# Kernel optimization log

Measured on AMD Instinct MI355X. Metric: run time of the kernel, lower is better.

## Reference

```python
import jax, jax.numpy as jnp
import numpy as np

D_MODEL = 256
NUM_LAYERS = 4
NUM_FREQ = 16
D_STATE = 8
NUM_HEADS = 4
LN_EPS = 1e-5


def setup_inputs() -> dict:
    key = jax.random.key(0)
    ks = jax.random.split(key, 30)
    B, NS, NQ = 16, 1024, 1024
    D, L, S = D_MODEL, NUM_LAYERS, D_STATE
    cin = 2 * NUM_FREQ + 1  # 33
    w = lambda k, shp, s=0.02: jax.random.normal(k, shp, dtype=jnp.float32) * s
    inp = {
        'sparse_coords': jax.random.uniform(ks[0], (B, NS, 2), minval=-1.0, maxval=1.0, dtype=jnp.float32),
        'sparse_values': jax.random.normal(ks[1], (B, NS, 1), dtype=jnp.float32),
        'query_coords': jax.random.uniform(ks[2], (B, NQ, 2), minval=-1.0, maxval=1.0, dtype=jnp.float32),
        't': jax.random.uniform(ks[3], (B,), dtype=jnp.float32),
        'noise': jax.random.normal(ks[4], (B, NQ, 1), dtype=jnp.float32),
        'B_f': jax.random.normal(ks[5], (2, NUM_FREQ), dtype=jnp.float32) * 10.0,
        'Wq_in': w(ks[6], (D, cin)), 'bq_in': jnp.zeros((D,), jnp.float32),
        'Wi_in': w(ks[7], (D, cin)), 'bi_in': jnp.zeros((D,), jnp.float32),
        'A_log': jax.random.normal(ks[8], (L, S), dtype=jnp.float32) * 0.1 - 1.0,
        'Bw': w(ks[9], (L, S, D)),
        'Cw': w(ks[10], (L, D, S)),
        'Dp': jax.random.normal(ks[11], (L, D), dtype=jnp.float32) * 0.01,
        'ln_g': jnp.ones((L, D), jnp.float32), 'ln_b': jnp.zeros((L, D), jnp.float32),
        'gate_w': w(ks[12], (L, D, D)), 'gate_b': jnp.zeros((L, D), jnp.float32),
        'in_proj_w': w(ks[13], (3 * D, D)), 'in_proj_b': jnp.zeros((3 * D,), jnp.float32),
        'out_w': w(ks[14], (D, D)), 'out_b': jnp.zeros((D,), jnp.float32),
        'dec_w1': w(ks[15], (D, D)), 'dec_b1': jnp.zeros((D,), jnp.float32),
        'dec_w2': w(ks[16], (1, D)), 'dec_b2': jnp.zeros((1,), jnp.float32),
    }
    return inp


def _layernorm(x, g, b):
    mu = jnp.mean(x, axis=-1, keepdims=True)
    var = jnp.mean(jnp.square(x - mu), axis=-1, keepdims=True)
    return (x - mu) * jax.lax.rsqrt(var + LN_EPS) * g + b


def _ssm(x, A_log, Bw, Cw, Dp):
    # x: (B, N, D)
    Bsz, N, D = x.shape
    A = -jnp.clip(jnp.exp(A_log), 1e-8, 10.0)          # (S,)
    A_bar = jnp.exp(A / N)                              # dt = 1/N
    Bu = jnp.einsum('bnd,sd->bns', x, Bw)               # (B, N, S)

    def step(h, bu_t):
        h = A_bar * h + bu_t
        return h, h

    h0 = jnp.zeros((Bsz, A_log.shape[0]), x.dtype)
    _, hs = jax.lax.scan(step, h0, jnp.swapaxes(Bu, 0, 1))  # (N, B, S)
    hs = jnp.swapaxes(hs, 0, 1)                             # (B, N, S)
    return jnp.einsum('bns,ds->bnd', hs, Cw) + Dp * x


def _time_embed(t, dim):
    half = dim // 2
    freqs = jnp.exp(jnp.arange(half, dtype=jnp.float32) * (-jnp.log(10000.0) / (half - 1)))
    emb = t[:, None] * freqs[None, :]
    return jnp.concatenate([jnp.sin(emb), jnp.cos(emb)], axis=-1)


def _fourier(coords, B_f):
    proj = coords @ B_f
    return jnp.concatenate([jnp.sin(proj), jnp.cos(proj)], axis=-1)


def reference(sparse_coords, sparse_values, query_coords, t, noise, B_f,
              Wq_in, bq_in, Wi_in, bi_in,
              A_log, Bw, Cw, Dp, ln_g, ln_b, gate_w, gate_b,
              in_proj_w, in_proj_b, out_w, out_b,
              dec_w1, dec_b1, dec_w2, dec_b2):
    D = D_MODEL
    NS = sparse_coords.shape[1]
    sparse_feats = _fourier(sparse_coords, B_f)
    query_feats = _fourier(query_coords, B_f)
    input_tokens = jnp.concatenate([sparse_feats, sparse_values], -1) @ Wi_in.T + bi_in
    query_tokens = jnp.concatenate([query_feats, noise], -1) @ Wq_in.T + bq_in
    t_emb = _time_embed(t, D)[:, None, :]
    seq = jnp.concatenate([input_tokens + t_emb, query_tokens + t_emb], axis=1)

    for l in range(A_log.shape[0]):
        xn = _layernorm(seq, ln_g[l], ln_b[l])
        gate = jax.nn.sigmoid(xn @ gate_w[l].T + gate_b[l])
        seq = seq + gate * _ssm(xn, A_log[l], Bw[l], Cw[l], Dp[l])

    input_seq = seq[:, :NS, :]
    query_seq = seq[:, NS:, :]

    # multi-head cross-attention (torch nn.MultiheadAttention semantics)
    H, hd = NUM_HEADS, D // NUM_HEADS
    q = query_seq @ in_proj_w[:D].T + in_proj_b[:D]
    k = input_seq @ in_proj_w[D:2 * D].T + in_proj_b[D:2 * D]
    v = input_seq @ in_proj_w[2 * D:].T + in_proj_b[2 * D:]
    def split(x):
        b, n, _ = x.shape
        return x.reshape(b, n, H, hd).transpose(0, 2, 1, 3)
    q, k, v = split(q), split(k), split(v)
    scores = jnp.einsum('bhqd,bhkd->bhqk', q, k) / jnp.sqrt(jnp.float32(hd))
    attn = jax.nn.softmax(scores, axis=-1)
    o = jnp.einsum('bhqk,bhkd->bhqd', attn, v)
    o = o.transpose(0, 2, 1, 3).reshape(query_seq.shape[0], -1, D)
    attended = o @ out_w.T + out_b

    h = jax.nn.relu(attended @ dec_w1.T + dec_b1)
    return h @ dec_w2.T + dec_b2
```

## Files before the change

kernel.cpp:

```cpp
#include <hip/hip_runtime.h>
#include <math.h>


typedef float floatx4 __attribute__((ext_vector_type(4)));
typedef short shortx8 __attribute__((ext_vector_type(8)));

__device__ __forceinline__ unsigned short f2bf(float f) {
  unsigned u = __builtin_bit_cast(unsigned, f);
  u += 0x7FFFu + ((u >> 16) & 1u);
  return (unsigned short)(u >> 16);
}
__device__ __forceinline__ float bf2f(unsigned short h) {
  unsigned u = ((unsigned)h) << 16;
  return __builtin_bit_cast(float, u);
}
__device__ __forceinline__ unsigned cvt_pk_bf16(float a, float b) {
  unsigned r;
  asm("v_cvt_pk_bf16_f32 %0, %1, %2" : "=v"(r) : "v"(a), "v"(b));
  return r;
}
__device__ __forceinline__ void split2(float f0, float f1, unsigned& ph, unsigned& pl) {
  ph = cvt_pk_bf16(f0, f1);
  float r0 = f0 - __builtin_bit_cast(float, ph << 16);
  float r1 = f1 - __builtin_bit_cast(float, ph & 0xFFFF0000u);
  pl = cvt_pk_bf16(r0, r1);
}
__device__ __forceinline__ void split8(float4 a, float4 b, uint4& uh, uint4& ul) {
  unsigned h0, h1, h2, h3, l0, l1, l2, l3;
  split2(a.x, a.y, h0, l0);
  split2(a.z, a.w, h1, l1);
  split2(b.x, b.y, h2, l2);
  split2(b.z, b.w, h3, l3);
  uh = make_uint4(h0, h1, h2, h3);
  ul = make_uint4(l0, l1, l2, l3);
}
__device__ __forceinline__ shortx8 lds_frag(const unsigned short* S, int row, int u) {
  uint4 v = *(const uint4*)(S + row * 64 + ((u ^ (row & 7)) << 3));
  return __builtin_bit_cast(shortx8, v);
}
__device__ __forceinline__ shortx8 lds_frag_v(const unsigned short* S, int row, int u) {
  uint4 v = *(const uint4*)(S + row * 64 + (((u ^ row ^ (row >> 3)) & 7) << 3));
  return __builtin_bit_cast(shortx8, v);
}
__device__ __forceinline__ shortx8 gfrag(const unsigned short* p) {
  return __builtin_bit_cast(shortx8, *(const uint4*)p);
}
__device__ __forceinline__ floatx4 mfma16(shortx8 a, shortx8 b, floatx4 c) {
  return __builtin_amdgcn_mfma_f32_16x16x32_bf16(a, b, c, 0, 0, 0);
}
__device__ __forceinline__ float wave_sum64(float v) {
#pragma unroll
  for (int m = 1; m < 64; m <<= 1) v += __shfl_xor(v, m);
  return v;
}

__global__ __launch_bounds__(256) void wconv_k(
    const float* __restrict__ gw, const float* __restrict__ ipw,
    const float* __restrict__ ow, const float* __restrict__ d1w,
    unsigned short* __restrict__ dh, unsigned short* __restrict__ dl) {
  int i = (blockIdx.x * 256 + threadIdx.x) * 8;
  const float* src;
  if (i < 262144) src = gw + i;
  else if (i < 458752) src = ipw + (i - 262144);
  else if (i < 524288) src = ow + (i - 458752);
  else src = d1w + (i - 524288);
  uint4 uh, ul;
  split8(*(const float4*)src, *(const float4*)(src + 4), uh, ul);
  *(uint4*)(dh + i) = uh;
  *(uint4*)(dl + i) = ul;
}

__global__ __launch_bounds__(256) void wconv2_k(
    const float* __restrict__ Wi, const float* __restrict__ Wq,
    unsigned short* __restrict__ eh, unsigned short* __restrict__ el) {
  int idx = blockIdx.x * 256 + threadIdx.x;
  int sel = idx >> 14, rem = idx & 16383;
  int row = rem >> 6, k = rem & 63;
  float v = 0.f;
  if (k < 33) v = (sel ? Wq : Wi)[row * 33 + k];
  unsigned short h = f2bf(v);
  eh[idx] = h;
  el[idx] = f2bf(v - bf2f(h));
}

__global__ __launch_bounds__(256) void embed_k(
    const float* __restrict__ sc, const float* __restrict__ sv,
    const float* __restrict__ qc, const float* __restrict__ tarr,
    const float* __restrict__ noise, const float* __restrict__ Bf,
    const float* __restrict__ bq, const float* __restrict__ bi,
    const unsigned short* __restrict__ Weh, const unsigned short* __restrict__ Wel,
    float* __restrict__ seq) {
  __shared__ unsigned short Ah[64 * 64];
  __shared__ unsigned short Al[64 * 64];
  __shared__ float teb[256];
  int tid = threadIdx.x;
  int bid = blockIdx.x;
  int chunk = bid & 15, half = (bid >> 4) & 1, b = bid >> 5;
  int rowbase = b * 2048 + half * 1024 + chunk * 64;
  {
    uint4 z = make_uint4(0, 0, 0, 0);
    *(uint4*)(Ah + tid * 8) = z;
    *(uint4*)(Ah + 2048 + tid * 8) = z;
    *(uint4*)(Al + tid * 8) = z;
    *(uint4*)(Al + 2048 + tid * 8) = z;
  }
  {
    float t = tarr[b];
    int dd = tid & 127;
    float e = t * __expf((float)dd * -0.07252236513367074f);
    float v = (tid < 128) ? sinf(e) : cosf(e);
    teb[tid] = v + (half ? bq : bi)[tid];
  }
  __syncthreads();
  {
    int tok = tid >> 2;
    int n = chunk * 64 + tok;
    const float* cp = (half ? qc : sc) + (size_t)(b * 1024 + n) * 2;
    float cx = cp[0], cy = cp[1];
#pragma unroll
    for (int jj = 0; jj < 4; ++jj) {
      int fr = (tid & 3) * 4 + jj;
      float px = cx * Bf[fr] + cy * Bf[16 + fr];
      float s = sinf(px), c = cosf(px);
      unsigned short sh = f2bf(s), ch = f2bf(c);
      int ks = fr, kc = 16 + fr;
      Ah[tok * 64 + (((ks >> 3) ^ (tok & 7)) << 3) + (ks & 7)] = sh;
      Al[tok * 64 + (((ks >> 3) ^ (tok & 7)) << 3) + (ks & 7)] = f2bf(s - bf2f(sh));
      Ah[tok * 64 + (((kc >> 3) ^ (tok & 7)) << 3) + (kc & 7)] = ch;
      Al[tok * 64 + (((kc >> 3) ^ (tok & 7)) << 3) + (kc & 7)] = f2bf(c - bf2f(ch));
    }
    if ((tid & 3) == 0) {
      float vv = (half ? noise : sv)[b * 1024 + n];
      unsigned short vh = f2bf(vv);
      Ah[tok * 64 + ((4 ^ (tok & 7)) << 3)] = vh;
      Al[tok * 64 + ((4 ^ (tok & 7)) << 3)] = f2bf(vv - bf2f(vh));
    }
  }
  __syncthreads();
  int w = tid >> 6, lane = tid & 63, lm = lane & 15, quad = lane >> 4;
  const unsigned short* Wb = Weh + half * 16384;
  const unsigned short* Wbl = Wel + half * 16384;
  floatx4 acc[4][4] = {};
#pragma unroll
  for (int s = 0; s < 2; ++s) {
    shortx8 afh[4], afl[4];
#pragma unroll
    for (int i = 0; i < 4; ++i) {
      afh[i] = lds_frag(Ah, i * 16 + lm, s * 4 + quad);
      afl[i] = lds_frag(Al, i * 16 + lm, s * 4 + quad);
    }
#pragma unroll
    for (int n = 0; n < 4; ++n) {
      int wr = w * 64 + n * 16 + lm;
      shortx8 bh = gfrag(Wb + wr * 64 + (s * 4 + quad) * 8);
      shortx8 bl = gfrag(Wbl + wr * 64 + (s * 4 + quad) * 8);
#pragma unroll
      for (int i = 0; i < 4; ++i) {
        acc[i][n] = mfma16(afl[i], bh, acc[i][n]);
        acc[i][n] = mfma16(afh[i], bl, acc[i][n]);
        acc[i][n] = mfma16(afh[i], bh, acc[i][n]);
      }
    }
  }
#pragma unroll
  for (int i = 0; i < 4; ++i)
#pragma unroll
    for (int n = 0; n < 4; ++n) {
      int col = w * 64 + n * 16 + lm;
      float te = teb[col];
#pragma unroll
      for (int r = 0; r < 4; ++r) {
        int tok = i * 16 + quad * 4 + r;
        seq[(size_t)(rowbase + tok) * 256 + col] = acc[i][n][r] + te;
      }
    }
}

__global__ __launch_bounds__(256) void scan_k(
    const float* __restrict__ BuT, const float* __restrict__ A_log,
    float* __restrict__ hsT) {
  int tid = threadIdx.x;
  int wid = blockIdx.x * 4 + (tid >> 6);
  int lane = tid & 63;
  int b = wid >> 3, s = wid & 7;
  float A = -fminf(fmaxf(expf(A_log[s]), 1e-8f), 10.0f);
  float abar = expf(A * (1.0f / 2048.0f));
  size_t base = (size_t)s * 32768 + b * 2048 + lane * 32;
  const float4* bu4 = (const float4*)(BuT + base);
  float4 v[8];
#pragma unroll
  for (int k = 0; k < 8; ++k) v[k] = bu4[k];
  float bl = 0.f;
#pragma unroll
  for (int k = 0; k < 8; ++k) {
    bl = abar * bl + v[k].x;
    bl = abar * bl + v[k].y;
    bl = abar * bl + v[k].z;
    bl = abar * bl + v[k].w;
  }
  float a = expf(A * (32.0f / 2048.0f));
  float bb = bl;
#pragma unroll
  for (int off = 1; off < 64; off <<= 1) {
    float pa = __shfl_up(a, (unsigned)off);
    float pb = __shfl_up(bb, (unsigned)off);
    if (lane >= off) { bb = a * pb + bb; a = a * pa; }
  }
  float h = __shfl_up(bb, 1u);
  if (lane == 0) h = 0.f;
  float4* hp4 = (float4*)(hsT + base);
#pragma unroll
  for (int k = 0; k < 8; ++k) {
    float h0 = abar * h + v[k].x;
    float h1 = abar * h0 + v[k].y;
    float h2 = abar * h1 + v[k].z;
    float h3 = abar * h2 + v[k].w;
    hp4[k] = make_float4(h0, h1, h2, h3);
    h = h3;
  }
}

template <int HASUPD>
__global__ __launch_bounds__(256, 2) void pe_k(
    float* __restrict__ seq, const float* __restrict__ Gprev,
    const float* __restrict__ hsTp, const float* __restrict__ CwP,
    const float* __restrict__ DpP, const float* __restrict__ gP,
    const float* __restrict__ bP, const float* __restrict__ gC,
    const float* __restrict__ bC, const float* __restrict__ BwL,
    const unsigned short* __restrict__ Wh, const unsigned short* __restrict__ Wl,
    const float* __restrict__ gbias, float* __restrict__ Gout,
    float* __restrict__ BuT) {
  __shared__ unsigned short slab[64 * 536];
  __shared__ float hsL[8 * 64];
  __shared__ float BwLds[8 * 256];
  int tid = threadIdx.x;
  int m0 = (int)blockIdx.x * 64;
  int w = tid >> 6, lane = tid & 63, lm = lane & 15, quad = lane >> 4;

#pragma unroll
  for (int j = 0; j < 8; ++j) BwLds[j * 256 + tid] = BwL[j * 256 + tid];
  if (HASUPD) {
    hsL[tid] = hsTp[(size_t)(tid >> 6) * 32768 + m0 + (tid & 63)];
    int v1 = tid + 256;
    hsL[v1] = hsTp[(size_t)(v1 >> 6) * 32768 + m0 + (v1 & 63)];
  }

  if (HASUPD) {
    __syncthreads();
    int c0 = lane * 4;
    float cw[4][8], dp4[4];
#pragma unroll
    for (int n = 0; n < 4; ++n) {
      float4 a0 = *(const float4*)(CwP + (size_t)(c0 + n) * 8);
      float4 a1 = *(const float4*)(CwP + (size_t)(c0 + n) * 8 + 4);
      cw[n][0] = a0.x; cw[n][1] = a0.y; cw[n][2] = a0.z; cw[n][3] = a0.w;
      cw[n][4] = a1.x; cw[n][5] = a1.y; cw[n][6] = a1.z; cw[n][7] = a1.w;
      dp4[n] = DpP[c0 + n];
    }
    float4 gg = *(const float4*)(gP + c0);
    float4 bb = *(const float4*)(bP + c0);
#pragma unroll
    for (int rr = 0; rr < 16; ++rr) {
      int r = w * 16 + rr;
      int row = m0 + r;
      float4 x = *(const float4*)(seq + (size_t)row * 256 + c0);
      float s1 = x.x + x.y + x.z + x.w;
      float s2 = x.x * x.x + x.y * x.y + x.z * x.z + x.w * x.w;
#pragma unroll
      for (int mk = 1; mk < 64; mk <<= 1) {
        s1 += __shfl_xor(s1, mk);
        s2 += __shfl_xor(s2, mk);
      }
      float mu = s1 * (1.0f / 256.0f);
      float var = s2 * (1.0f / 256.0f) - mu * mu;
      float rs = rsqrtf(var + 1e-5f);
      float xn0 = (x.x - mu) * rs * gg.x + bb.x;
      float xn1 = (x.y - mu) * rs * gg.y + bb.y;
      float xn2 = (x.z - mu) * rs * gg.z + bb.z;
      float xn3 = (x.w - mu) * rs * gg.w + bb.w;
      float hv[8];
#pragma unroll
      for (int s = 0; s < 8; ++s) hv[s] = hsL[s * 64 + r];
      float y0 = dp4[0] * xn0, y1 = dp4[1] * xn1, y2 = dp4[2] * xn2, y3 = dp4[3] * xn3;
#pragma unroll
      for (int s = 0; s < 8; ++s) {
        y0 += hv[s] * cw[0][s];
        y1 += hv[s] * cw[1][s];
        y2 += hv[s] * cw[2][s];
        y3 += hv[s] * cw[3][s];
      }
      float4 gp = *(const float4*)(Gprev + (size_t)row * 256 + c0);
      x.x += gp.x * y0; x.y += gp.y * y1; x.z += gp.z * y2; x.w += gp.w * y3;
      *(float4*)(seq + (size_t)row * 256 + c0) = x;
      *(float4*)((char*)slab + (size_t)r * 1072 + c0 * 4) = x;
    }
    __syncthreads();
  }

  {
    int r = tid >> 2, q2 = tid & 3;
    int row = m0 + r;
    float4 xr[16];
#pragma unroll
    for (int j = 0; j < 16; ++j) {
      if (HASUPD)
        xr[j] = *(const float4*)((const char*)slab + (size_t)r * 1072 + (q2 * 64 + j * 4) * 4);
      else
        xr[j] = *(const float4*)(seq + (size_t)row * 256 + q2 * 64 + j * 4);
    }
    __syncthreads();
    float s1 = 0.f, s2 = 0.f;
#pragma unroll
    for (int j = 0; j < 16; ++j) {
      s1 += (xr[j].x + xr[j].y) + (xr[j].z + xr[j].w);
      s2 += (xr[j].x * xr[j].x + xr[j].y * xr[j].y) + (xr[j].z * xr[j].z + xr[j].w * xr[j].w);
    }
    s1 += __shfl_xor(s1, 1); s2 += __shfl_xor(s2, 1);
    s1 += __shfl_xor(s1, 2); s2 += __shfl_xor(s2, 2);
    float mu = s1 * (1.0f / 256.0f);
    float var = s2 * (1.0f / 256.0f) - mu * mu;
    float rs = rsqrtf(var + 1e-5f);
    float bu[8] = {};
#pragma unroll
    for (int j = 0; j < 16; ++j) {
      int c = q2 * 64 + j * 4;
      float4 gg = *(const float4*)(gC + c);
      float4 bb = *(const float4*)(bC + c);
      float4 xn;
      xn.x = (xr[j].x - mu) * rs * gg.x + bb.x;
      xn.y = (xr[j].y - mu) * rs * gg.y + bb.y;
      xn.z = (xr[j].z - mu) * rs * gg.z + bb.z;
      xn.w = (xr[j].w - mu) * rs * gg.w + bb.w;
#pragma unroll
      for (int s = 0; s < 8; ++s) {
        const float4 bw = *(const float4*)(BwLds + s * 256 + c);
        bu[s] += (xn.x * bw.x + xn.y * bw.y) + (xn.z * bw.z + xn.w * bw.w);
      }
      unsigned h0, l0, h1, l1;
      split2(xn.x, xn.y, h0, l0);
      split2(xn.z, xn.w, h1, l1);
      *(uint2*)((char*)slab + (size_t)r * 1072 + c * 2) = make_uint2(h0, h1);
      *(uint2*)((char*)slab + (size_t)r * 1072 + 512 + c * 2) = make_uint2(l0, l1);
    }
#pragma unroll
    for (int s = 0; s < 8; ++s) {
      bu[s] += __shfl_xor(bu[s], 1);
      bu[s] += __shfl_xor(bu[s], 2);
    }
    if (q2 == 0) {
#pragma unroll
      for (int s = 0; s < 8; ++s) BuT[(size_t)s * 32768 + row] = bu[s];
    }
  }
  __syncthreads();

  floatx4 acc[4][4] = {};
  {
    uint4 wa[8], wb[8];
    const size_t wcbase = (size_t)(w * 64 + lm) * 256 + quad * 8;
#pragma unroll
    for (int n = 0; n < 4; ++n) {
      wa[n * 2]     = *(const uint4*)(Wh + wcbase + (size_t)n * 16 * 256);
      wa[n * 2 + 1] = *(const uint4*)(Wl + wcbase + (size_t)n * 16 * 256);
    }
#pragma unroll
    for (int ku = 0; ku < 8; ++ku) {
      uint4* cur = (ku & 1) ? wb : wa;
      uint4* nxt = (ku & 1) ? wa : wb;
      if (ku < 7) {
        size_t koff = wcbase + (size_t)(ku + 1) * 32;
#pragma unroll
        for (int n = 0; n < 4; ++n) {
          nxt[n * 2]     = *(const uint4*)(Wh + koff + (size_t)n * 16 * 256);
          nxt[n * 2 + 1] = *(const uint4*)(Wl + koff + (size_t)n * 16 * 256);
        }
      }
      int slot = ku * 4 + quad;
      shortx8 afh[4], afl[4];
#pragma unroll
      for (int m = 0; m < 4; ++m) {
        const char* rb = (const char*)slab + (size_t)(m * 16 + lm) * 1072;
        afh[m] = __builtin_bit_cast(shortx8, *(const uint4*)(rb + slot * 16));
        afl[m] = __builtin_bit_cast(shortx8, *(const uint4*)(rb + 512 + slot * 16));
      }
#pragma unroll
      for (int m = 0; m < 4; ++m)
#pragma unroll
        for (int n = 0; n < 4; ++n) {
          shortx8 bh = __builtin_bit_cast(shortx8, cur[n * 2]);
          shortx8 bl = __builtin_bit_cast(shortx8, cur[n * 2 + 1]);
          acc[m][n] = mfma16(afl[m], bh, acc[m][n]);
          acc[m][n] = mfma16(afh[m], bl, acc[m][n]);
          acc[m][n] = mfma16(afh[m], bh, acc[m][n]);
        }
    }
  }
  float bi4[4];
#pragma unroll
  for (int n = 0; n < 4; ++n) bi4[n] = gbias[w * 64 + n * 16 + lm];
#pragma unroll
  for (int m = 0; m < 4; ++m)
#pragma unroll
    for (int r = 0; r < 4; ++r) {
      int row = m0 + m * 16 + quad * 4 + r;
#pragma unroll
      for (int n = 0; n < 4; ++n) {
        int col = w * 64 + n * 16 + lm;
        float v = acc[m][n][r] + bi4[n];
        Gout[(size_t)row * 256 + col] = 1.0f / (1.0f + __expf(-v));
      }
    }
}

__global__ __launch_bounds__(256) void upd_k(
    float* __restrict__ seq, const float* __restrict__ G,
    const float* __restrict__ hsT, const float* __restrict__ Cw,
    const float* __restrict__ Dp, const float* __restrict__ g,
    const float* __restrict__ be) {
  int tid = threadIdx.x;
  int row = blockIdx.x * 4 + (tid >> 6);
  int lane = tid & 63;
  int c0 = lane * 4;
  float4 x = *(const float4*)(seq + (size_t)row * 256 + c0);
  float s1 = x.x + x.y + x.z + x.w;
  float s2 = x.x * x.x + x.y * x.y + x.z * x.z + x.w * x.w;
#pragma unroll
  for (int mk = 1; mk < 64; mk <<= 1) {
    s1 += __shfl_xor(s1, mk);
    s2 += __shfl_xor(s2, mk);
  }
  float mu = s1 * (1.0f / 256.0f);
  float var = s2 * (1.0f / 256.0f) - mu * mu;
  float rs = rsqrtf(var + 1e-5f);
  float4 gg = *(const float4*)(g + c0);
  float4 bb = *(const float4*)(be + c0);
  float xn0 = (x.x - mu) * rs * gg.x + bb.x;
  float xn1 = (x.y - mu) * rs * gg.y + bb.y;
  float xn2 = (x.z - mu) * rs * gg.z + bb.z;
  float xn3 = (x.w - mu) * rs * gg.w + bb.w;
  float hv[8];
#pragma unroll
  for (int s = 0; s < 8; ++s) hv[s] = hsT[(size_t)s * 32768 + row];
  float y0, y1, y2, y3;
  {
    float4 d = *(const float4*)(Dp + c0);
    y0 = d.x * xn0; y1 = d.y * xn1; y2 = d.z * xn2; y3 = d.w * xn3;
  }
#pragma unroll
  for (int n = 0; n < 4; ++n) {
    float4 a0 = *(const float4*)(Cw + (size_t)(c0 + n) * 8);
    float4 a1 = *(const float4*)(Cw + (size_t)(c0 + n) * 8 + 4);
    float yn = hv[0] * a0.x + hv[1] * a0.y + hv[2] * a0.z + hv[3] * a0.w +
               hv[4] * a1.x + hv[5] * a1.y + hv[6] * a1.z + hv[7] * a1.w;
    if (n == 0) y0 += yn;
    else if (n == 1) y1 += yn;
    else if (n == 2) y2 += yn;
    else y3 += yn;
  }
  float4 gp = *(const float4*)(G + (size_t)row * 256 + c0);
  x.x += gp.x * y0; x.y += gp.y * y1; x.z += gp.z * y2; x.w += gp.w * y3;
  *(float4*)(seq + (size_t)row * 256 + c0) = x;
}

template <int NPASS>
__global__ __launch_bounds__(256, 2) void proj_k(
    const float* __restrict__ src, const unsigned short* __restrict__ Wh,
    const unsigned short* __restrict__ Wl, const float* __restrict__ bias,
    unsigned short* __restrict__ Ch, unsigned short* __restrict__ Cl,
    int ldc, int aBase) {
  __shared__ unsigned short slab[32 * 536];
  int tid = threadIdx.x;
  int m0 = (int)blockIdx.x * 32;
  int w = tid >> 6, lane = tid & 63, lm = lane & 15, quad = lane >> 4;
  {
    int r = tid >> 3, q8 = tid & 7;
    int am = m0 + r;
    int garow = ((am >> 10) * 2048) + aBase + (am & 1023);
    const float* sp = src + (size_t)garow * 256 + q8 * 32;
    char* rb = (char*)slab + (size_t)r * 1072;
#pragma unroll
    for (int j = 0; j < 8; ++j) {
      float4 x = *(const float4*)(sp + j * 4);
      unsigned h0, l0, h1, l1;
      split2(x.x, x.y, h0, l0);
      split2(x.z, x.w, h1, l1);
      int c = q8 * 32 + j * 4;
      *(uint2*)(rb + c * 2) = make_uint2(h0, h1);
      *(uint2*)(rb + 512 + c * 2) = make_uint2(l0, l1);
    }
  }
  __syncthreads();
#pragma unroll
  for (int cp = 0; cp < NPASS; ++cp) {
    floatx4 acc[2][4] = {};
    {
      uint4 wa[8], wb[8];
      const size_t wcbase = (size_t)(cp * 256 + w * 64 + lm) * 256 + quad * 8;
#pragma unroll
      for (int n = 0; n < 4; ++n) {
        wa[n * 2]     = *(const uint4*)(Wh + wcbase + (size_t)n * 16 * 256);
        wa[n * 2 + 1] = *(const uint4*)(Wl + wcbase + (size_t)n * 16 * 256);
      }
#pragma unroll
      for (int ku = 0; ku < 8; ++ku) {
        uint4* cur = (ku & 1) ? wb : wa;
        uint4* nxt = (ku & 1) ? wa : wb;
        if (ku < 7) {
          size_t koff = wcbase + (size_t)(ku + 1) * 32;
#pragma unroll
          for (int n = 0; n < 4; ++n) {
            nxt[n * 2]     = *(const uint4*)(Wh + koff + (size_t)n * 16 * 256);
            nxt[n * 2 + 1] = *(const uint4*)(Wl + koff + (size_t)n * 16 * 256);
          }
        }
        int slot = ku * 4 + quad;
        shortx8 afh[2], afl[2];
#pragma unroll
        for (int m = 0; m < 2; ++m) {
          const char* rb = (const char*)slab + (size_t)(m * 16 + lm) * 1072;
          afh[m] = __builtin_bit_cast(shortx8, *(const uint4*)(rb + slot * 16));
          afl[m] = __builtin_bit_cast(shortx8, *(const uint4*)(rb + 512 + slot * 16));
        }
#pragma unroll
        for (int m = 0; m < 2; ++m)
#pragma unroll
          for (int n = 0; n < 4; ++n) {
            shortx8 bh = __builtin_bit_cast(shortx8, cur[n * 2]);
            shortx8 bl = __builtin_bit_cast(shortx8, cur[n * 2 + 1]);
            acc[m][n] = mfma16(afl[m], bh, acc[m][n]);
            acc[m][n] = mfma16(afh[m], bl, acc[m][n]);
            acc[m][n] = mfma16(afh[m], bh, acc[m][n]);
          }
      }
    }
    float bi4[4];
#pragma unroll
    for (int n = 0; n < 4; ++n) bi4[n] = bias[cp * 256 + w * 64 + n * 16 + lm];
#pragma unroll
    for (int m = 0; m < 2; ++m)
#pragma unroll
      for (int r = 0; r < 4; ++r) {
        int row = m0 + m * 16 + quad * 4 + r;
        size_t ro = (size_t)row * ldc + cp * 256;
#pragma unroll
        for (int np = 0; np < 2; ++np) {
          int colA = w * 64 + (2 * np) * 16 + lm;
          float vA = acc[m][2 * np][r] + bi4[2 * np];
          float vB = acc[m][2 * np + 1][r] + bi4[2 * np + 1];
          unsigned ph, pl;
          split2(vA, vB, ph, pl);
          Ch[ro + colA] = (unsigned short)ph;
          Ch[ro + colA + 16] = (unsigned short)(ph >> 16);
          Cl[ro + colA] = (unsigned short)pl;
          Cl[ro + colA + 16] = (unsigned short)(pl >> 16);
        }
      }
  }
}

__global__ __launch_bounds__(256, 2) void dec_k(
    const float* __restrict__ src, const unsigned short* __restrict__ W1h,
    const unsigned short* __restrict__ W1l, const float* __restrict__ b1,
    const unsigned short* __restrict__ W2h, const unsigned short* __restrict__ W2l,
    const float* __restrict__ b2v, const float* __restrict__ w2,
    const float* __restrict__ b2, float* __restrict__ out) {
  __shared__ unsigned short slab[32 * 536];
  __shared__ float pw[4][32];
  int tid = threadIdx.x;
  int m0 = (int)blockIdx.x * 32;
  int w = tid >> 6, lane = tid & 63, lm = lane & 15, quad = lane >> 4;
  {
    int r = tid >> 3, q8 = tid & 7;
    const float* sp = src + (size_t)(m0 + r) * 256 + q8 * 32;
    char* rb = (char*)slab + (size_t)r * 1072;
#pragma unroll
    for (int j = 0; j < 8; ++j) {
      float4 x = *(const float4*)(sp + j * 4);
      unsigned h0, l0, h1, l1;
      split2(x.x, x.y, h0, l0);
      split2(x.z, x.w, h1, l1);
      int c = q8 * 32 + j * 4;
      *(uint2*)(rb + c * 2) = make_uint2(h0, h1);
      *(uint2*)(rb + 512 + c * 2) = make_uint2(l0, l1);
    }
  }
  __syncthreads();
  floatx4 acc[2][4] = {};
  {
    uint4 wa[8], wb[8];
    const size_t wcbase = (size_t)(w * 64 + lm) * 256 + quad * 8;
#pragma unroll
    for (int n = 0; n < 4; ++n) {
      wa[n * 2]     = *(const uint4*)(W1h + wcbase + (size_t)n * 16 * 256);
      wa[n * 2 + 1] = *(const uint4*)(W1l + wcbase + (size_t)n * 16 * 256);
    }
#pragma unroll
    for (int ku = 0; ku < 8; ++ku) {
      uint4* cur = (ku & 1) ? wb : wa;
      uint4* nxt = (ku & 1) ? wa : wb;
      if (ku < 7) {
        size_t koff = wcbase + (size_t)(ku + 1) * 32;
#pragma unroll
        for (int n = 0; n < 4; ++n) {
          nxt[n * 2]     = *(const uint4*)(W1h + koff + (size_t)n * 16 * 256);
          nxt[n * 2 + 1] = *(const uint4*)(W1l + koff + (size_t)n * 16 * 256);
        }
      }
      int slot = ku * 4 + quad;
      shortx8 afh[2], afl[2];
#pragma unroll
      for (int m = 0; m < 2; ++m) {
        const char* rb = (const char*)slab + (size_t)(m * 16 + lm) * 1072;
        afh[m] = __builtin_bit_cast(shortx8, *(const uint4*)(rb + slot * 16));
        afl[m] = __builtin_bit_cast(shortx8, *(const uint4*)(rb + 512 + slot * 16));
      }
#pragma unroll
      for (int m = 0; m < 2; ++m)
#pragma unroll
        for (int n = 0; n < 4; ++n) {
          shortx8 bh = __builtin_bit_cast(shortx8, cur[n * 2]);
          shortx8 bl = __builtin_bit_cast(shortx8, cur[n * 2 + 1]);
          acc[m][n] = mfma16(afl[m], bh, acc[m][n]);
          acc[m][n] = mfma16(afh[m], bl, acc[m][n]);
          acc[m][n] = mfma16(afh[m], bh, acc[m][n]);
        }
    }
  }
  __syncthreads();
  {
    float bi4[4];
#pragma unroll
    for (int n = 0; n < 4; ++n) bi4[n] = b1[w * 64 + n * 16 + lm];
#pragma unroll
    for (int m = 0; m < 2; ++m)
#pragma unroll
      for (int r = 0; r < 4; ++r) {
        int rr = m * 16 + quad * 4 + r;
        char* rb = (char*)slab + (size_t)rr * 1072;
#pragma unroll
        for (int np = 0; np < 2; ++np) {
          int cA = w * 64 + (2 * np) * 16 + lm;
          int cB = cA + 16;
          float vA = acc[m][2 * np][r] + bi4[2 * np];
          float vB = acc[m][2 * np + 1][r] + bi4[2 * np + 1];
          unsigned ph, pl;
          split2(vA, vB, ph, pl);
          *(unsigned short*)(rb + cA * 2) = (unsigned short)ph;
          *(unsigned short*)(rb + cB * 2) = (unsigned short)(ph >> 16);
          *(unsigned short*)(rb + 512 + cA * 2) = (unsigned short)pl;
          *(unsigned short*)(rb + 512 + cB * 2) = (unsigned short)(pl >> 16);
        }
      }
  }
  __syncthreads();
  floatx4 acc2[2][4] = {};
  {
    uint4 wa[8], wb[8];
    const size_t wcbase = (size_t)(w * 64 + lm) * 256 + quad * 8;
#pragma unroll
    for (int n = 0; n < 4; ++n) {
      wa[n * 2]     = *(const uint4*)(W2h + wcbase + (size_t)n * 16 * 256);
      wa[n * 2 + 1] = *(const uint4*)(W2l + wcbase + (size_t)n * 16 * 256);
    }
#pragma unroll
    for (int ku = 0; ku < 8; ++ku) {
      uint4* cur = (ku & 1) ? wb : wa;
      uint4* nxt = (ku & 1) ? wa : wb;
      if (ku < 7) {
        size_t koff = wcbase + (size_t)(ku + 1) * 32;
#pragma unroll
        for (int n = 0; n < 4; ++n) {
          nxt[n * 2]     = *(const uint4*)(W2h + koff + (size_t)n * 16 * 256);
          nxt[n * 2 + 1] = *(const uint4*)(W2l + koff + (size_t)n * 16 * 256);
        }
      }
      int slot = ku * 4 + quad;
      shortx8 afh[2], afl[2];
#pragma unroll
      for (int m = 0; m < 2; ++m) {
        const char* rb = (const char*)slab + (size_t)(m * 16 + lm) * 1072;
        afh[m] = __builtin_bit_cast(shortx8, *(const uint4*)(rb + slot * 16));
        afl[m] = __builtin_bit_cast(shortx8, *(const uint4*)(rb + 512 + slot * 16));
      }
#pragma unroll
      for (int m = 0; m < 2; ++m)
#pragma unroll
        for (int n = 0; n < 4; ++n) {
          shortx8 bh = __builtin_bit_cast(shortx8, cur[n * 2]);
          shortx8 bl = __builtin_bit_cast(shortx8, cur[n * 2 + 1]);
          acc2[m][n] = mfma16(afl[m], bh, acc2[m][n]);
          acc2[m][n] = mfma16(afh[m], bl, acc2[m][n]);
          acc2[m][n] = mfma16(afh[m], bh, acc2[m][n]);
        }
    }
  }
  {
    float b14[4], w24[4];
#pragma unroll
    for (int n = 0; n < 4; ++n) {
      int col = w * 64 + n * 16 + lm;
      b14[n] = b2v[col];
      w24[n] = w2[col];
    }
#pragma unroll
    for (int m = 0; m < 2; ++m)
#pragma unroll
      for (int r = 0; r < 4; ++r) {
        float p = 0.f;
#pragma unroll
        for (int n = 0; n < 4; ++n) {
          float hvv = fmaxf(acc2[m][n][r] + b14[n], 0.0f);
          p += hvv * w24[n];
        }
        p += __shfl_xor(p, 1);
        p += __shfl_xor(p, 2);
        p += __shfl_xor(p, 4);
        p += __shfl_xor(p, 8);
        if (lm == 0) pw[w][m * 16 + quad * 4 + r] = p;
      }
  }
  __syncthreads();
  if (tid < 32)
    out[m0 + tid] = pw[0][tid] + pw[1][tid] + pw[2][tid] + pw[3][tid] + b2[0];
}

__global__ __launch_bounds__(256, 2) void attn_k(
    const unsigned short* __restrict__ qh, const unsigned short* __restrict__ ql,
    const unsigned short* __restrict__ kvh, const unsigned short* __restrict__ kvl,
    float* __restrict__ ob) {
  __shared__ unsigned short Ksh[2][64 * 64];
  __shared__ unsigned short Ksl[2][64 * 64];
  __shared__ unsigned short Vt[2][64 * 64];
  __shared__ unsigned short Ps[4 * 16 * 64];
  int tid = threadIdx.x;
  int bid = blockIdx.x;
  int bh = bid & 63, qt = bid >> 6;
  int h = bh & 3, b = bh >> 2;
  int w = tid >> 6, lane = tid & 63, lm = lane & 15, quad = lane >> 4;
  int sr = tid >> 3, scu = tid & 7;
  unsigned short* Pw = Ps + w * 1024;
  shortx8 qfh[2], qfl[2];
  {
    size_t qoff = (size_t)(b * 1024 + qt * 64 + w * 16 + lm) * 256 + h * 64;
#pragma unroll
    for (int s = 0; s < 2; ++s) {
      qfh[s] = gfrag(qh + qoff + s * 32 + quad * 8);
      qfl[s] = gfrag(ql + qoff + s * 32 + quad * 8);
    }
  }
  float lac = 0.f;
  floatx4 oacc[4] = {};
  const size_t kvbase = ((size_t)(b * 1024)) * 512 + h * 64;
  const float sc_l2 = 0.125f * 1.44269504089f;
  int vg = tid & 7, vk = (tid >> 3) * 2;
  uint4 kh4[2], kl4[2], vv0, vv1;
  auto load_kv = [&](int kt) {
#pragma unroll
    for (int p = 0; p < 2; ++p) {
      int r = sr + p * 32;
      size_t a = kvbase + (size_t)(kt * 64 + r) * 512 + scu * 8;
      kh4[p] = *(const uint4*)(kvh + a);
      kl4[p] = *(const uint4*)(kvl + a);
    }
    vv0 = *(const uint4*)(kvh + kvbase + (size_t)(kt * 64 + vk) * 512 + 256 + vg * 8);
    vv1 = *(const uint4*)(kvh + kvbase + (size_t)(kt * 64 + vk + 1) * 512 + 256 + vg * 8);
  };
  const int kt0 = qt & 15;
  load_kv(kt0);
  for (int it = 0; it < 16; ++it) {
    int cur = it & 1;
    unsigned short* KshC = Ksh[cur];
    unsigned short* KslC = Ksl[cur];
    unsigned short* VtC = Vt[cur];
#pragma unroll
    for (int p = 0; p < 2; ++p) {
      int r = sr + p * 32;
      int off = r * 64 + ((scu ^ (r & 7)) << 3);
      *(uint4*)(KshC + off) = kh4[p];
      *(uint4*)(KslC + off) = kl4[p];
    }
    {
      shortx8 s0 = __builtin_bit_cast(shortx8, vv0);
      shortx8 s1 = __builtin_bit_cast(shortx8, vv1);
      unsigned short* vb = VtC + vg * 512 + (vk & 7);
      int x0 = ((vk >> 3) ^ vg) & 7;
#pragma unroll
      for (int j = 0; j < 8; ++j) {
        unsigned pack = ((unsigned)(unsigned short)s0[j]) |
                        (((unsigned)(unsigned short)s1[j]) << 16);
        *(unsigned*)(vb + j * 64 + ((x0 ^ j) << 3)) = pack;
      }
    }
    __syncthreads();
    if (it < 15) load_kv((kt0 + it + 1) & 15);
    floatx4 sacc[4] = {};
#pragma unroll
    for (int s = 0; s < 2; ++s) {
#pragma unroll
      for (int m = 0; m < 4; ++m) {
        shortx8 kfh = lds_frag(KshC, m * 16 + lm, s * 4 + quad);
        shortx8 kfl = lds_frag(KslC, m * 16 + lm, s * 4 + quad);
        sacc[m] = mfma16(kfl, qfh[s], sacc[m]);
        sacc[m] = mfma16(kfh, qfl[s], sacc[m]);
        sacc[m] = mfma16(kfh, qfh[s], sacc[m]);
      }
    }
#pragma unroll
    for (int m = 0; m < 4; ++m) {
      float p0 = exp2f(sacc[m][0] * sc_l2 - 12.0f);
      float p1 = exp2f(sacc[m][1] * sc_l2 - 12.0f);
      float p2 = exp2f(sacc[m][2] * sc_l2 - 12.0f);
      float p3 = exp2f(sacc[m][3] * sc_l2 - 12.0f);
      lac += (p0 + p1) + (p2 + p3);
      int u = (m * 2 + (quad >> 1)) ^ (lm & 7);
      unsigned short* base = Pw + lm * 64 + u * 8 + (quad & 1) * 4;
      *(uint2*)base = make_uint2(cvt_pk_bf16(p0, p1), cvt_pk_bf16(p2, p3));
    }
#pragma unroll
    for (int s = 0; s < 2; ++s) {
      shortx8 pf = lds_frag(Pw, lm, s * 4 + quad);
#pragma unroll
      for (int n = 0; n < 4; ++n) {
        shortx8 vf = lds_frag_v(VtC, n * 16 + lm, s * 4 + quad);
        oacc[n] = mfma16(pf, vf, oacc[n]);
      }
    }
  }
  lac += __shfl_xor(lac, 16);
  lac += __shfl_xor(lac, 32);
  const size_t obase = ((size_t)(b * 1024 + qt * 64 + w * 16)) * 256 + h * 64;
#pragma unroll
  for (int r = 0; r < 4; ++r) {
    int row = quad * 4 + r;
    float inv = 1.0f / __shfl(lac, row);
#pragma unroll
    for (int n = 0; n < 4; ++n)
      ob[obase + (size_t)row * 256 + n * 16 + lm] = oacc[n][r] * inv;
  }
}

extern "C" void kernel_launch(void* const* d_in, const int* in_sizes, int n_in,
                              void* d_out, int out_size, void* d_ws, size_t ws_size,
                              hipStream_t stream) {
  const float* sparse_coords = (const float*)d_in[0];
  const float* sparse_values = (const float*)d_in[1];
  const float* query_coords  = (const float*)d_in[2];
  const float* t_arr         = (const float*)d_in[3];
  const float* noise         = (const float*)d_in[4];
  const float* B_f           = (const float*)d_in[5];
  const float* Wq_in         = (const float*)d_in[6];
  const float* bq_in         = (const float*)d_in[7];
  const float* Wi_in         = (const float*)d_in[8];
  const float* bi_in         = (const float*)d_in[9];
  const float* A_log         = (const float*)d_in[10];
  const float* Bw            = (const float*)d_in[11];
  const float* Cw            = (const float*)d_in[12];
  const float* Dp            = (const float*)d_in[13];
  const float* ln_g          = (const float*)d_in[14];
  const float* ln_b          = (const float*)d_in[15];
  const float* gate_w        = (const float*)d_in[16];
  const float* gate_b        = (const float*)d_in[17];
  const float* in_proj_w     = (const float*)d_in[18];
  const float* in_proj_b     = (const float*)d_in[19];
  const float* out_w         = (const float*)d_in[20];
  const float* out_b         = (const float*)d_in[21];
  const float* dec_w1        = (const float*)d_in[22];
  const float* dec_b1        = (const float*)d_in[23];
  const float* dec_w2        = (const float*)d_in[24];
  const float* dec_b2        = (const float*)d_in[25];

  unsigned short* us = (unsigned short*)d_ws;
  float* seq = (float*)us;
  float* G = (float*)(us + 16777216);
  unsigned short* qhp = us + 33554432;
  unsigned short* qlp = qhp + 4194304;
  unsigned short* kvh = qlp + 4194304;
  unsigned short* kvl = kvh + 8388608;
  float* BuT = (float*)(kvl + 8388608);
  float* hsT = BuT + 262144;
  unsigned short* whi = (unsigned short*)(hsT + 262144);
  unsigned short* wlo = whi + 589824;
  unsigned short* Weh = wlo + 589824;
  unsigned short* Wel = Weh + 32768;
  float* obuf = G;

  wconv_k<<<288, 256, 0, stream>>>(gate_w, in_proj_w, out_w, dec_w1, whi, wlo);
  wconv2_k<<<128, 256, 0, stream>>>(Wi_in, Wq_in, Weh, Wel);
  embed_k<<<512, 256, 0, stream>>>(sparse_coords, sparse_values, query_coords,
                                   t_arr, noise, B_f, bq_in, bi_in, Weh, Wel, seq);
  pe_k<0><<<512, 256, 0, stream>>>(seq, nullptr, nullptr, nullptr, nullptr,
                                   nullptr, nullptr, ln_g, ln_b, Bw,
                                   whi, wlo, gate_b, G, BuT);
  scan_k<<<32, 256, 0, stream>>>(BuT, A_log, hsT);
  for (int l = 1; l < 4; ++l) {
    pe_k<1><<<512, 256, 0, stream>>>(
        seq, G, hsT, Cw + (l - 1) * 2048, Dp + (l - 1) * 256,
        ln_g + (l - 1) * 256, ln_b + (l - 1) * 256,
        ln_g + l * 256, ln_b + l * 256, Bw + l * 2048,
        whi + l * 65536, wlo + l * 65536, gate_b + l * 256, G, BuT);
    scan_k<<<32, 256, 0, stream>>>(BuT, A_log + l * 8, hsT);
  }
  upd_k<<<8192, 256, 0, stream>>>(seq, G, hsT, Cw + 3 * 2048, Dp + 3 * 256,
                                  ln_g + 768, ln_b + 768);
  proj_k<1><<<512, 256, 0, stream>>>(seq, whi + 262144, wlo + 262144,
                                     in_proj_b, qhp, qlp, 256, 1024);
  proj_k<2><<<512, 256, 0, stream>>>(seq, whi + 327680, wlo + 327680,
                                     in_proj_b + 256, kvh, kvl, 512, 0);
  attn_k<<<1024, 256, 0, stream>>>(qhp, qlp, kvh, kvl, obuf);
  dec_k<<<512, 256, 0, stream>>>(obuf, whi + 458752, wlo + 458752, out_b,
                                 whi + 524288, wlo + 524288, dec_b1, dec_w2,
                                 dec_b2, (float*)d_out);
}
```

Baseline: 513.5 us.

## Merge Q/K/V projections into one launch and pass attention P via shuffles

The two projection launches (Q with one pass, KV with two passes) become one kernel with 1536 blocks, each block computing a single 256-column sector. This exposes more parallelism and removes a launch, at the cost of re-staging the activation rows per sector. In attention, the P tile no longer goes through LDS: the bf16-packed probabilities are rearranged into the MFMA A-fragment layout with cross-lane shuffles. That frees LDS, and launch bounds are raised to 3 blocks per CU to try for higher occupancy, though register pressure may limit it.

```diff
diff --git a/kernel.cpp b/kernel.cpp
--- a/kernel.cpp
+++ b/kernel.cpp
@@ -462,15 +462,24 @@
   *(float4*)(seq + (size_t)row * 256 + c0) = x;
 }
 
-template <int NPASS>
-__global__ __launch_bounds__(256, 2) void proj_k(
-    const float* __restrict__ src, const unsigned short* __restrict__ Wh,
-    const unsigned short* __restrict__ Wl, const float* __restrict__ bias,
-    unsigned short* __restrict__ Ch, unsigned short* __restrict__ Cl,
-    int ldc, int aBase) {
+__global__ __launch_bounds__(256, 2) void proj3_k(
+    const float* __restrict__ src, const unsigned short* __restrict__ Whb,
+    const unsigned short* __restrict__ Wlb, const float* __restrict__ biasb,
+    unsigned short* __restrict__ qhp, unsigned short* __restrict__ qlp,
+    unsigned short* __restrict__ kvh, unsigned short* __restrict__ kvl) {
   __shared__ unsigned short slab[32 * 536];
   int tid = threadIdx.x;
-  int m0 = (int)blockIdx.x * 32;
+  int bid = (int)blockIdx.x;
+  int sector = bid >> 9, blk = bid & 511;
+  int m0 = blk * 32;
+  int aBase = (sector == 0) ? 1024 : 0;
+  const unsigned short* Wh = Whb + (size_t)sector * 65536;
+  const unsigned short* Wl = Wlb + (size_t)sector * 65536;
+  const float* bias = biasb + sector * 256;
+  unsigned short* Ch = (sector == 0) ? qhp : kvh;
+  unsigned short* Cl = (sector == 0) ? qlp : kvl;
+  int ldc = (sector == 0) ? 256 : 512;
+  int colOff = (sector == 2) ? 256 : 0;
   int w = tid >> 6, lane = tid & 63, lm = lane & 15, quad = lane >> 4;
   {
     int r = tid >> 3, q8 = tid & 7;
@@ -490,72 +499,69 @@
     }
   }
   __syncthreads();
-#pragma unroll
-  for (int cp = 0; cp < NPASS; ++cp) {
-    floatx4 acc[2][4] = {};
-    {
-      uint4 wa[8], wb[8];
-      const size_t wcbase = (size_t)(cp * 256 + w * 64 + lm) * 256 + quad * 8;
-#pragma unroll
-      for (int n = 0; n < 4; ++n) {
-        wa[n * 2]     = *(const uint4*)(Wh + wcbase + (size_t)n * 16 * 256);
-        wa[n * 2 + 1] = *(const uint4*)(Wl + wcbase + (size_t)n * 16 * 256);
-      }
-#pragma unroll
-      for (int ku = 0; ku < 8; ++ku) {
-        uint4* cur = (ku & 1) ? wb : wa;
-        uint4* nxt = (ku & 1) ? wa : wb;
-        if (ku < 7) {
-          size_t koff = wcbase + (size_t)(ku + 1) * 32;
-#pragma unroll
-          for (int n = 0; n < 4; ++n) {
-            nxt[n * 2]     = *(const uint4*)(Wh + koff + (size_t)n * 16 * 256);
-            nxt[n * 2 + 1] = *(const uint4*)(Wl + koff + (size_t)n * 16 * 256);
-          }
+  floatx4 acc[2][4] = {};
+  {
+    uint4 wa[8], wb[8];
+    const size_t wcbase = (size_t)(w * 64 + lm) * 256 + quad * 8;
+#pragma unroll
+    for (int n = 0; n < 4; ++n) {
+      wa[n * 2]     = *(const uint4*)(Wh + wcbase + (size_t)n * 16 * 256);
+      wa[n * 2 + 1] = *(const uint4*)(Wl + wcbase + (size_t)n * 16 * 256);
+    }
+#pragma unroll
+    for (int ku = 0; ku < 8; ++ku) {
+      uint4* cur = (ku & 1) ? wb : wa;
+      uint4* nxt = (ku & 1) ? wa : wb;
+      if (ku < 7) {
+        size_t koff = wcbase + (size_t)(ku + 1) * 32;
+#pragma unroll
+        for (int n = 0; n < 4; ++n) {
+          nxt[n * 2]     = *(const uint4*)(Wh + koff + (size_t)n * 16 * 256);
+          nxt[n * 2 + 1] = *(const uint4*)(Wl + koff + (size_t)n * 16 * 256);
         }
-        int slot = ku * 4 + quad;
-        shortx8 afh[2], afl[2];
-#pragma unroll
-        for (int m = 0; m < 2; ++m) {
-          const char* rb = (const char*)slab + (size_t)(m * 16 + lm) * 1072;
-          afh[m] = __builtin_bit_cast(shortx8, *(const uint4*)(rb + slot * 16));
-          afl[m] = __builtin_bit_cast(shortx8, *(const uint4*)(rb + 512 + slot * 16));
+      }
+      int slot = ku * 4 + quad;
+      shortx8 afh[2], afl[2];
+#pragma unroll
+      for (int m = 0; m < 2; ++m) {
+        const char* rb = (const char*)slab + (size_t)(m * 16 + lm) * 1072;
+        afh[m] = __builtin_bit_cast(shortx8, *(const uint4*)(rb + slot * 16));
+        afl[m] = __builtin_bit_cast(shortx8, *(const uint4*)(rb + 512 + slot * 16));
+      }
+#pragma unroll
+      for (int m = 0; m < 2; ++m)
+#pragma unroll
+        for (int n = 0; n < 4; ++n) {
+          shortx8 bh = __builtin_bit_cast(shortx8, cur[n * 2]);
+          shortx8 bl = __builtin_bit_cast(shortx8, cur[n * 2 + 1]);
+          acc[m][n] = mfma16(afl[m], bh, acc[m][n]);
+          acc[m][n] = mfma16(afh[m], bl, acc[m][n]);
+          acc[m][n] = mfma16(afh[m], bh, acc[m][n]);
         }
-#pragma unroll
-        for (int m = 0; m < 2; ++m)
-#pragma unroll
-          for (int n = 0; n < 4; ++n) {
-            shortx8 bh = __builtin_bit_cast(shortx8, cur[n * 2]);
-            shortx8 bl = __builtin_bit_cast(shortx8, cur[n * 2 + 1]);
-            acc[m][n] = mfma16(afl[m], bh, acc[m][n]);
-            acc[m][n] = mfma16(afh[m], bl, acc[m][n]);
-            acc[m][n] = mfma16(afh[m], bh, acc[m][n]);
-          }
-      }
-    }
-    float bi4[4];
-#pragma unroll
-    for (int n = 0; n < 4; ++n) bi4[n] = bias[cp * 256 + w * 64 + n * 16 + lm];
-#pragma unroll
-    for (int m = 0; m < 2; ++m)
-#pragma unroll
-      for (int r = 0; r < 4; ++r) {
-        int row = m0 + m * 16 + quad * 4 + r;
-        size_t ro = (size_t)row * ldc + cp * 256;
-#pragma unroll
-        for (int np = 0; np < 2; ++np) {
-          int colA = w * 64 + (2 * np) * 16 + lm;
-          float vA = acc[m][2 * np][r] + bi4[2 * np];
-          float vB = acc[m][2 * np + 1][r] + bi4[2 * np + 1];
-          unsigned ph, pl;
-          split2(vA, vB, ph, pl);
-          Ch[ro + colA] = (unsigned short)ph;
-          Ch[ro + colA + 16] = (unsigned short)(ph >> 16);
-          Cl[ro + colA] = (unsigned short)pl;
-          Cl[ro + colA + 16] = (unsigned short)(pl >> 16);
-        }
-      }
-  }
+    }
+  }
+  float bi4[4];
+#pragma unroll
+  for (int n = 0; n < 4; ++n) bi4[n] = bias[w * 64 + n * 16 + lm];
+#pragma unroll
+  for (int m = 0; m < 2; ++m)
+#pragma unroll
+    for (int r = 0; r < 4; ++r) {
+      int row = m0 + m * 16 + quad * 4 + r;
+      size_t ro = (size_t)row * ldc + colOff;
+#pragma unroll
+      for (int np = 0; np < 2; ++np) {
+        int colA = w * 64 + (2 * np) * 16 + lm;
+        float vA = acc[m][2 * np][r] + bi4[2 * np];
+        float vB = acc[m][2 * np + 1][r] + bi4[2 * np + 1];
+        unsigned ph, pl;
+        split2(vA, vB, ph, pl);
+        Ch[ro + colA] = (unsigned short)ph;
+        Ch[ro + colA + 16] = (unsigned short)(ph >> 16);
+        Cl[ro + colA] = (unsigned short)pl;
+        Cl[ro + colA + 16] = (unsigned short)(pl >> 16);
+      }
+    }
 }
 
 __global__ __launch_bounds__(256, 2) void dec_k(
@@ -724,21 +730,19 @@
     out[m0 + tid] = pw[0][tid] + pw[1][tid] + pw[2][tid] + pw[3][tid] + b2[0];
 }
 
-__global__ __launch_bounds__(256, 2) void attn_k(
+__global__ __launch_bounds__(256, 3) void attn_k(
     const unsigned short* __restrict__ qh, const unsigned short* __restrict__ ql,
     const unsigned short* __restrict__ kvh, const unsigned short* __restrict__ kvl,
     float* __restrict__ ob) {
   __shared__ unsigned short Ksh[2][64 * 64];
   __shared__ unsigned short Ksl[2][64 * 64];
   __shared__ unsigned short Vt[2][64 * 64];
-  __shared__ unsigned short Ps[4 * 16 * 64];
   int tid = threadIdx.x;
   int bid = blockIdx.x;
   int bh = bid & 63, qt = bid >> 6;
   int h = bh & 3, b = bh >> 2;
   int w = tid >> 6, lane = tid & 63, lm = lane & 15, quad = lane >> 4;
   int sr = tid >> 3, scu = tid & 7;
-  unsigned short* Pw = Ps + w * 1024;
   shortx8 qfh[2], qfl[2];
   {
     size_t qoff = (size_t)(b * 1024 + qt * 64 + w * 16 + lm) * 256 + h * 64;
@@ -767,6 +771,8 @@
   };
   const int kt0 = qt & 15;
   load_kv(kt0);
+  const int src0 = lm + ((quad & 1) << 5);
+  const int src1 = src0 + 16;
   for (int it = 0; it < 16; ++it) {
     int cur = it & 1;
     unsigned short* KshC = Ksh[cur];
@@ -805,6 +811,7 @@
         sacc[m] = mfma16(kfh, qfh[s], sacc[m]);
       }
     }
+    unsigned pk[4][2];
 #pragma unroll
     for (int m = 0; m < 4; ++m) {
       float p0 = exp2f(sacc[m][0] * sc_l2 - 12.0f);
@@ -812,13 +819,21 @@
       float p2 = exp2f(sacc[m][2] * sc_l2 - 12.0f);
       float p3 = exp2f(sacc[m][3] * sc_l2 - 12.0f);
       lac += (p0 + p1) + (p2 + p3);
-      int u = (m * 2 + (quad >> 1)) ^ (lm & 7);
-      unsigned short* base = Pw + lm * 64 + u * 8 + (quad & 1) * 4;
-      *(uint2*)base = make_uint2(cvt_pk_bf16(p0, p1), cvt_pk_bf16(p2, p3));
+      pk[m][0] = cvt_pk_bf16(p0, p1);
+      pk[m][1] = cvt_pk_bf16(p2, p3);
     }
 #pragma unroll
     for (int s = 0; s < 2; ++s) {
-      shortx8 pf = lds_frag(Pw, lm, s * 4 + quad);
+      unsigned lo0 = pk[s * 2][0], lo1 = pk[s * 2][1];
+      unsigned hi0 = pk[s * 2 + 1][0], hi1 = pk[s * 2 + 1][1];
+      unsigned b00 = __shfl(lo0, src0), b01 = __shfl(lo1, src0);
+      unsigned b02 = __shfl(lo0, src1), b03 = __shfl(lo1, src1);
+      unsigned b10 = __shfl(hi0, src0), b11 = __shfl(hi1, src0);
+      unsigned b12 = __shfl(hi0, src1), b13 = __shfl(hi1, src1);
+      bool sel = (quad & 2) != 0;
+      uint4 pv = make_uint4(sel ? b10 : b00, sel ? b11 : b01,
+                            sel ? b12 : b02, sel ? b13 : b03);
+      shortx8 pf = __builtin_bit_cast(shortx8, pv);
 #pragma unroll
       for (int n = 0; n < 4; ++n) {
         shortx8 vf = lds_frag_v(VtC, n * 16 + lm, s * 4 + quad);
@@ -902,10 +917,8 @@
   }
   upd_k<<<8192, 256, 0, stream>>>(seq, G, hsT, Cw + 3 * 2048, Dp + 3 * 256,
                                   ln_g + 768, ln_b + 768);
-  proj_k<1><<<512, 256, 0, stream>>>(seq, whi + 262144, wlo + 262144,
-                                     in_proj_b, qhp, qlp, 256, 1024);
-  proj_k<2><<<512, 256, 0, stream>>>(seq, whi + 327680, wlo + 327680,
-                                     in_proj_b + 256, kvh, kvl, 512, 0);
+  proj3_k<<<1536, 256, 0, stream>>>(seq, whi + 262144, wlo + 262144,
+                                    in_proj_b, qhp, qlp, kvh, kvl);
   attn_k<<<1024, 256, 0, stream>>>(qhp, qlp, kvh, kvl, obuf);
   dec_k<<<512, 256, 0, stream>>>(obuf, whi + 458752, wlo + 458752, out_b,
                                  whi + 524288, wlo + 524288, dec_b1, dec_w2,
```

Result: slower. 527.6 us (+2.7%).
